# Kernel optimization log

Hardware: AMD Instinct MI355X
Metric: run time of the kernel (lower is better)

Reference implementation:

```python
import jax, jax.numpy as jnp
import numpy as np

EPS = 1e-5
QB = 127.0  # int8 activation quantization bound

def rmsnorm(x):
    # SimpleRMSNorm: x / rms(x), no learned scale
    return x * jax.lax.rsqrt(jnp.mean(x * x, axis=-1, keepdims=True) + EPS)

def activation_quant(x):
    # per-token absmax int8 quant-dequant
    scale = QB / jnp.clip(jnp.max(jnp.abs(x), axis=-1, keepdims=True), EPS)
    return jnp.clip(jnp.round(x * scale), -QB - 1, QB) / scale

def weight_quant(w):
    # per-tensor ternary quant-dequant (BitNet b1.58)
    scale = 1.0 / jnp.clip(jnp.mean(jnp.abs(w)), EPS)
    return jnp.clip(jnp.round(w * scale), -1.0, 1.0) / scale

def ste(x, q):
    # straight-through estimator: forward uses q, gradient flows to x
    return x + jax.lax.stop_gradient(q - x)

def bitlinear(x, w, b):
    xn = rmsnorm(x)
    xq = ste(xn, activation_quant(xn))
    wq = ste(w, weight_quant(w))
    # x: [b, s, d_in], w: [d_out, d_in] -> [b, s, d_out]
    return jnp.einsum('bsd,od->bso', xq, wq) + b

def setup_inputs() -> dict:
    key = jax.random.key(0)
    k1, k2, k3, k4, k5 = jax.random.split(key, 5)
    dim, inner = 1024, 4096
    x = jax.random.normal(k1, (4, 4096, dim), dtype=jnp.float32)
    w1 = jax.random.normal(k2, (inner, dim), dtype=jnp.float32) * (dim ** -0.5)
    b1 = jax.random.normal(k3, (inner,), dtype=jnp.float32) * 0.02
    w2 = jax.random.normal(k4, (dim, inner), dtype=jnp.float32) * (inner ** -0.5)
    b2 = jax.random.normal(k5, (dim,), dtype=jnp.float32) * 0.02
    return {"x": x, "w1": w1, "b1": b1, "w2": w2, "b2": b2}

def reference(x, w1, b1, w2, b2):
    h = jax.nn.gelu(bitlinear(x, w1, b1), approximate=False)  # torch nn.GELU default = exact erf
    # dropout p=0.0 is identity; post_act_ln disabled
    return bitlinear(h, w2, b2)
```

## Files before the change

### kernel.cpp

```cpp
#include <hip/hip_runtime.h>
#include <hip/hip_bf16.h>

#define TOK   16384
#define DIM   1024
#define INNER 4096
#define EPSF  1e-5f

typedef int v4i __attribute__((ext_vector_type(4)));

static __device__ __forceinline__ void async_copy16(const char* g, char* l) {
    __builtin_amdgcn_global_load_lds(
        (const __attribute__((address_space(1))) unsigned int*)g,
        (__attribute__((address_space(3))) unsigned int*)l, 16, 0, 0);
}

static __device__ __forceinline__ float bf2f(unsigned short u) {
    return __uint_as_float(((unsigned)u) << 16);
}
static __device__ __forceinline__ unsigned short f2bf(float f) {
    unsigned u = __float_as_uint(f);
    return (unsigned short)((u + 0x7fffu + ((u >> 16) & 1u)) >> 16);
}

static __device__ __forceinline__ float waveSum(float v) {
#pragma unroll
    for (int o = 32; o > 0; o >>= 1) v += __shfl_down(v, o, 64);
    return v;
}
static __device__ __forceinline__ float waveMax(float v) {
#pragma unroll
    for (int o = 32; o > 0; o >>= 1) v = fmaxf(v, __shfl_down(v, o, 64));
    return v;
}

__global__ void absmean_k(const float* __restrict__ w, int n4, float* __restrict__ acc) {
    int idx = blockIdx.x * blockDim.x + threadIdx.x;
    int stride = gridDim.x * blockDim.x;
    const float4* w4 = (const float4*)w;
    float s = 0.f;
    for (int i = idx; i < n4; i += stride) {
        float4 v = w4[i];
        s += fabsf(v.x) + fabsf(v.y) + fabsf(v.z) + fabsf(v.w);
    }
    __shared__ float sp[4];
    int wv = threadIdx.x >> 6, lane = threadIdx.x & 63;
    s = waveSum(s);
    if (lane == 0) sp[wv] = s;
    __syncthreads();
    if (threadIdx.x == 0) atomicAdd(acc, sp[0] + sp[1] + sp[2] + sp[3]);
}

__global__ void wquant_k(const float* __restrict__ w, int n,
                         const float* __restrict__ acc, float* __restrict__ wscale,
                         char* __restrict__ wq) {
    float mean = *acc / (float)n;
    float cl = fmaxf(mean, EPSF);
    float s = 1.f / cl;
    if (blockIdx.x == 0 && threadIdx.x == 0) *wscale = cl;
    int idx = blockIdx.x * blockDim.x + threadIdx.x;
    int stride = gridDim.x * blockDim.x;
    int n4 = n >> 2;
    const float4* w4 = (const float4*)w;
    unsigned* q4 = (unsigned*)wq;
    for (int i = idx; i < n4; i += stride) {
        float4 v = w4[i];
        float e[4] = {v.x, v.y, v.z, v.w};
        unsigned packed = 0;
#pragma unroll
        for (int j = 0; j < 4; j++) {
            float r = rintf(e[j] * s);
            r = fminf(fmaxf(r, -1.f), 1.f);
            packed |= ((unsigned)((int)r & 0xff)) << (8 * j);
        }
        q4[i] = packed;
    }
}

template <int D, int VPT>
__global__ void actquant_f32_k(const float* __restrict__ X, char* __restrict__ Q,
                               float* __restrict__ rs_out) {
    int token = blockIdx.x;
    int t = threadIdx.x;
    const float4* xp = (const float4*)(X + (long)token * D);
    float vals[VPT];
    float ss = 0.f, am = 0.f;
#pragma unroll
    for (int j = 0; j < VPT / 4; j++) {
        float4 v = xp[t * (VPT / 4) + j];
        vals[4 * j] = v.x; vals[4 * j + 1] = v.y; vals[4 * j + 2] = v.z; vals[4 * j + 3] = v.w;
        ss += v.x * v.x + v.y * v.y + v.z * v.z + v.w * v.w;
        am = fmaxf(am, fmaxf(fmaxf(fabsf(v.x), fabsf(v.y)), fmaxf(fabsf(v.z), fabsf(v.w))));
    }
    __shared__ float sp[8];
    __shared__ float bc[2];
    int wv = t >> 6, lane = t & 63;
    float S = waveSum(ss);
    float M = waveMax(am);
    if (lane == 0) { sp[wv] = S; sp[4 + wv] = M; }
    __syncthreads();
    if (t == 0) {
        float Sa = sp[0] + sp[1] + sp[2] + sp[3];
        float Ma = fmaxf(fmaxf(sp[4], sp[5]), fmaxf(sp[6], sp[7]));
        float rinv = rsqrtf(Sa * (1.f / (float)D) + EPSF);
        float amn = Ma * rinv;
        float scale = 127.f / fmaxf(amn, EPSF);
        rs_out[token] = 1.f / scale;
        bc[0] = rinv; bc[1] = scale;
    }
    __syncthreads();
    float rinv = bc[0], scale = bc[1];
    unsigned outw[VPT / 4];
#pragma unroll
    for (int j = 0; j < VPT; j++) {
        float r = rintf((vals[j] * rinv) * scale);
        r = fminf(fmaxf(r, -128.f), 127.f);
        unsigned qi = (unsigned)((int)r & 0xff) << (8 * (j & 3));
        if ((j & 3) == 0) outw[j / 4] = qi; else outw[j / 4] |= qi;
    }
    unsigned* qp = (unsigned*)(Q + (long)token * D);
#pragma unroll
    for (int j = 0; j < VPT / 4; j++) qp[t * (VPT / 4) + j] = outw[j];
}

template <int D, int VPT>
__global__ void actquant_bf16_k(const unsigned short* __restrict__ X, char* __restrict__ Q,
                                float* __restrict__ rs_out) {
    int token = blockIdx.x;
    int t = threadIdx.x;
    const unsigned* x2 = (const unsigned*)(X + (long)token * D);
    float vals[VPT];
    float ss = 0.f, am = 0.f;
#pragma unroll
    for (int j = 0; j < VPT / 2; j++) {
        unsigned v = x2[t * (VPT / 2) + j];
        float f0 = bf2f((unsigned short)(v & 0xffff));
        float f1 = bf2f((unsigned short)(v >> 16));
        vals[2 * j] = f0; vals[2 * j + 1] = f1;
        ss += f0 * f0 + f1 * f1;
        am = fmaxf(am, fmaxf(fabsf(f0), fabsf(f1)));
    }
    __shared__ float sp[8];
    __shared__ float bc[2];
    int wv = t >> 6, lane = t & 63;
    float S = waveSum(ss);
    float M = waveMax(am);
    if (lane == 0) { sp[wv] = S; sp[4 + wv] = M; }
    __syncthreads();
    if (t == 0) {
        float Sa = sp[0] + sp[1] + sp[2] + sp[3];
        float Ma = fmaxf(fmaxf(sp[4], sp[5]), fmaxf(sp[6], sp[7]));
        float rinv = rsqrtf(Sa * (1.f / (float)D) + EPSF);
        float amn = Ma * rinv;
        float scale = 127.f / fmaxf(amn, EPSF);
        rs_out[token] = 1.f / scale;
        bc[0] = rinv; bc[1] = scale;
    }
    __syncthreads();
    float rinv = bc[0], scale = bc[1];
    unsigned outw[VPT / 4];
#pragma unroll
    for (int j = 0; j < VPT; j++) {
        float r = rintf((vals[j] * rinv) * scale);
        r = fminf(fmaxf(r, -128.f), 127.f);
        unsigned qi = (unsigned)((int)r & 0xff) << (8 * (j & 3));
        if ((j & 3) == 0) outw[j / 4] = qi; else outw[j / 4] |= qi;
    }
    unsigned* qp = (unsigned*)(Q + (long)token * D);
#pragma unroll
    for (int j = 0; j < VPT / 4; j++) qp[t * (VPT / 4) + j] = outw[j];
}

template <int DO_GELU, int OUT_F32>
__global__ __launch_bounds__(256) void gemm_i8_k(
    const char* __restrict__ A, const char* __restrict__ Bw,
    const float* __restrict__ rs, const float* __restrict__ wscale_p,
    const float* __restrict__ bias, void* __restrict__ outp,
    int M, int N, int K) {
    __shared__ char As[8192];
    __shared__ char Bs[8192];
    int t = threadIdx.x;
    int n0 = blockIdx.x * 128, m0 = blockIdx.y * 128;
    int wv = t >> 6, lane = t & 63, lm = lane & 15, q = lane >> 4;
    int wrow = (wv >> 1) * 64, wcol = (wv & 1) * 64;

    int r = t >> 2;
    int csrc = (t & 3) ^ (r & 3);
    const char* Ap = A + (long)(m0 + r) * K + csrc * 16;
    const char* Bp = Bw + (long)(n0 + r) * K + csrc * 16;
    long rowoff = (long)64 * K;

    v4i acc[4][4] = {};
    const v4i* As4 = (const v4i*)As;
    const v4i* Bs4 = (const v4i*)Bs;
    int aidx[4], bidx[4];
#pragma unroll
    for (int i = 0; i < 4; i++) {
        int ml = wrow + i * 16 + lm;
        aidx[i] = ml * 4 + (q ^ (ml & 3));
        int nl = wcol + i * 16 + lm;
        bidx[i] = nl * 4 + (q ^ (nl & 3));
    }

    for (int k0 = 0; k0 < K; k0 += 64) {
        async_copy16(Ap + k0,          As + t * 16);
        async_copy16(Ap + rowoff + k0, As + 4096 + t * 16);
        async_copy16(Bp + k0,          Bs + t * 16);
        async_copy16(Bp + rowoff + k0, Bs + 4096 + t * 16);
        __syncthreads();
        v4i a[4], b[4];
#pragma unroll
        for (int i = 0; i < 4; i++) { a[i] = As4[aidx[i]]; b[i] = Bs4[bidx[i]]; }
#pragma unroll
        for (int i = 0; i < 4; i++)
#pragma unroll
            for (int j = 0; j < 4; j++)
                acc[i][j] = __builtin_amdgcn_mfma_i32_16x16x64_i8(a[i], b[j], acc[i][j], 0, 0, 0);
        __syncthreads();
    }

    float wsc = *wscale_p;
#pragma unroll
    for (int i = 0; i < 4; i++) {
        int mg = m0 + wrow + i * 16 + q * 4;
        float fs[4];
#pragma unroll
        for (int rr = 0; rr < 4; rr++) fs[rr] = rs[mg + rr] * wsc;
#pragma unroll
        for (int j = 0; j < 4; j++) {
            int ng = n0 + wcol + j * 16 + lm;
            float bv = bias[ng];
#pragma unroll
            for (int rr = 0; rr < 4; rr++) {
                float v = (float)acc[i][j][rr] * fs[rr] + bv;
                if (DO_GELU) v = 0.5f * v * (1.f + erff(v * 0.70710678118654752f));
                long idx = (long)(mg + rr) * N + ng;
                if (OUT_F32) ((float*)outp)[idx] = v;
                else ((unsigned short*)outp)[idx] = f2bf(v);
            }
        }
    }
}

extern "C" void kernel_launch(void* const* d_in, const int* in_sizes, int n_in,
                              void* d_out, int out_size, void* d_ws, size_t ws_size,
                              hipStream_t stream) {
    const float* x  = (const float*)d_in[0];
    const float* w1 = (const float*)d_in[1];
    const float* b1 = (const float*)d_in[2];
    const float* w2 = (const float*)d_in[3];
    const float* b2 = (const float*)d_in[4];
    float* out = (float*)d_out;

    char* ws = (char*)d_ws;
    float* acc1 = (float*)(ws + 0);
    float* acc2 = (float*)(ws + 4);
    float* wsc1 = (float*)(ws + 8);
    float* wsc2 = (float*)(ws + 12);
    size_t off = 256;
    char* w1q = ws + off; off += (size_t)INNER * DIM;
    char* w2q = ws + off; off += (size_t)INNER * DIM;
    char* xq1 = ws + off; off += (size_t)TOK * DIM;
    float* rs1 = (float*)(ws + off); off += (size_t)TOK * 4;
    char* xq2 = ws + off; off += (size_t)TOK * INNER;
    float* rs2 = (float*)(ws + off); off += (size_t)TOK * 4;
    unsigned short* h = (unsigned short*)(ws + off);

    hipMemsetAsync(d_ws, 0, 16, stream);

    int nw = INNER * DIM;
    absmean_k<<<1024, 256, 0, stream>>>(w1, nw / 4, acc1);
    absmean_k<<<1024, 256, 0, stream>>>(w2, nw / 4, acc2);
    wquant_k<<<2048, 256, 0, stream>>>(w1, nw, acc1, wsc1, w1q);
    wquant_k<<<2048, 256, 0, stream>>>(w2, nw, acc2, wsc2, w2q);

    actquant_f32_k<DIM, 4><<<TOK, 256, 0, stream>>>(x, xq1, rs1);
    gemm_i8_k<1, 0><<<dim3(INNER / 128, TOK / 128), 256, 0, stream>>>(
        xq1, w1q, rs1, wsc1, b1, (void*)h, TOK, INNER, DIM);
    actquant_bf16_k<INNER, 16><<<TOK, 256, 0, stream>>>(h, xq2, rs2);
    gemm_i8_k<0, 1><<<dim3(DIM / 128, TOK / 128), 256, 0, stream>>>(
        xq2, w2q, rs2, wsc2, b2, (void*)out, TOK, DIM, INNER);
}
```

Measured before the change: 465.0 us.

## Double-buffer int8 GEMM LDS tiles and use polynomial erf approximation for GELU

Adds two LDS buffers per operand in the int8 MFMA GEMM so the async global-to-LDS load of the next K-tile overlaps MFMA work on the current one. The wait uses an explicit vmcnt count and raw s_barrier in place of __syncthreads. Separately, it swaps erff in the GELU epilogue for an Abramowitz-Stegun polynomial with fast exp and rcp. The GELU change cuts epilogue arithmetic at the cost of about 1e-7 absolute erf error. LDS use doubles to 32KB per block, which may lower occupancy, and the hand-written waitcnt/barrier sequence depends on the compiler's vmcnt bookkeeping.

```diff
diff --git a/kernel.cpp b/kernel.cpp
--- a/kernel.cpp
+++ b/kernel.cpp
@@ -20,6 +20,15 @@
 static __device__ __forceinline__ unsigned short f2bf(float f) {
     unsigned u = __float_as_uint(f);
     return (unsigned short)((u + 0x7fffu + ((u >> 16) & 1u)) >> 16);
+}
+
+static __device__ __forceinline__ float fast_erf(float z) {
+    float az = fabsf(z);
+    float tt = __builtin_amdgcn_rcpf(1.f + 0.3275911f * az);
+    float poly = ((((1.061405429f * tt - 1.453152027f) * tt + 1.421413741f) * tt
+                   - 0.284496736f) * tt + 0.254829592f) * tt;
+    float er = 1.f - poly * __expf(-az * az);
+    return copysignf(er, z);
 }
 
 static __device__ __forceinline__ float waveSum(float v) {
@@ -176,8 +185,8 @@
     const float* __restrict__ rs, const float* __restrict__ wscale_p,
     const float* __restrict__ bias, void* __restrict__ outp,
     int M, int N, int K) {
-    __shared__ char As[8192];
-    __shared__ char Bs[8192];
+    __shared__ char As[2][8192];
+    __shared__ char Bs[2][8192];
     int t = threadIdx.x;
     int n0 = blockIdx.x * 128, m0 = blockIdx.y * 128;
     int wv = t >> 6, lane = t & 63, lm = lane & 15, q = lane >> 4;
@@ -190,8 +199,6 @@
     long rowoff = (long)64 * K;
 
     v4i acc[4][4] = {};
-    const v4i* As4 = (const v4i*)As;
-    const v4i* Bs4 = (const v4i*)Bs;
     int aidx[4], bidx[4];
 #pragma unroll
     for (int i = 0; i < 4; i++) {
@@ -201,12 +208,27 @@
         bidx[i] = nl * 4 + (q ^ (nl & 3));
     }
 
-    for (int k0 = 0; k0 < K; k0 += 64) {
-        async_copy16(Ap + k0,          As + t * 16);
-        async_copy16(Ap + rowoff + k0, As + 4096 + t * 16);
-        async_copy16(Bp + k0,          Bs + t * 16);
-        async_copy16(Bp + rowoff + k0, Bs + 4096 + t * 16);
-        __syncthreads();
+    auto issue = [&](int it, int buf) {
+        long k0 = (long)it << 6;
+        async_copy16(Ap + k0,          As[buf] + t * 16);
+        async_copy16(Ap + rowoff + k0, As[buf] + 4096 + t * 16);
+        async_copy16(Bp + k0,          Bs[buf] + t * 16);
+        async_copy16(Bp + rowoff + k0, Bs[buf] + 4096 + t * 16);
+    };
+
+    int nIt = K >> 6;
+    issue(0, 0);
+    for (int it = 0; it < nIt; ++it) {
+        int cur = it & 1;
+        if (it + 1 < nIt) {
+            issue(it + 1, cur ^ 1);
+            asm volatile("s_waitcnt vmcnt(4)" ::: "memory");
+        } else {
+            asm volatile("s_waitcnt vmcnt(0)" ::: "memory");
+        }
+        asm volatile("s_barrier" ::: "memory");
+        const v4i* As4 = (const v4i*)As[cur];
+        const v4i* Bs4 = (const v4i*)Bs[cur];
         v4i a[4], b[4];
 #pragma unroll
         for (int i = 0; i < 4; i++) { a[i] = As4[aidx[i]]; b[i] = Bs4[bidx[i]]; }
@@ -215,7 +237,7 @@
 #pragma unroll
             for (int j = 0; j < 4; j++)
                 acc[i][j] = __builtin_amdgcn_mfma_i32_16x16x64_i8(a[i], b[j], acc[i][j], 0, 0, 0);
-        __syncthreads();
+        asm volatile("s_barrier" ::: "memory");
     }
 
     float wsc = *wscale_p;
@@ -232,7 +254,7 @@
 #pragma unroll
             for (int rr = 0; rr < 4; rr++) {
                 float v = (float)acc[i][j][rr] * fs[rr] + bv;
-                if (DO_GELU) v = 0.5f * v * (1.f + erff(v * 0.70710678118654752f));
+                if (DO_GELU) v = 0.5f * v * (1.f + fast_erf(v * 0.70710678118654752f));
                 long idx = (long)(mg + rr) * N + ng;
                 if (OUT_F32) ((float*)outp)[idx] = v;
                 else ((unsigned short*)outp)[idx] = f2bf(v);
```

New measurement: 440.0 us. 1.06x faster.
